# Performance work log

Measured on AMD Instinct MI355X. Metric: run time of the kernel, lower is better.

## Reference

```python
import jax, jax.numpy as jnp
import numpy as np


def setup_inputs() -> dict:
    key = jax.random.key(0)
    k = jax.random.split(key, 6)
    E, F_len, B, r = 64, 128, 1024, 16
    E2 = E * E
    hid = max(1, E2 // r)
    return {
        "mu": jax.random.normal(k[0], (5, B, E, F_len), dtype=jnp.float32),
        "A": jax.random.uniform(k[1], (E, E), dtype=jnp.float32),
        "W1": jax.random.normal(k[2], (hid, E2), dtype=jnp.float32) * 0.02,
        "W2": jax.random.normal(k[3], (E2, hid), dtype=jnp.float32) * 0.02,
        "T1": jax.random.normal(k[4], (5, F_len, F_len), dtype=jnp.float32) * 0.01,
        "T2": jax.random.normal(k[5], (5, F_len, F_len), dtype=jnp.float32) * 0.01,
    }


def reference(mu, A, W1, W2, T1, T2):
    E = A.shape[0]
    # dynamic adjacency: squeeze-excite on flattened A (Linear has no bias)
    h = jax.nn.elu(A.reshape(-1) @ W1.T)          # [E2//r]
    Ad = jax.nn.relu(h @ W2.T).reshape(E, E)       # [E, E]
    # diag(1/rowsum) @ Ad == row-wise normalization (same math, O(E^2))
    D_invA = Ad / jnp.maximum(Ad.sum(axis=1, keepdims=True), 1e-6)
    # per-band chain, vectorized over the 5 bands: elu(D_invA @ elu(m @ T1) @ T2)
    h1 = jax.nn.elu(jnp.einsum('gbef,gfh->gbeh', mu, T1))   # [5,B,E,F]
    h2 = jnp.einsum('xe,gbeh->gbxh', D_invA, h1)            # [5,B,E,F]
    out = jax.nn.elu(jnp.einsum('gbeh,ghf->gbef', h2, T2))  # [5,B,E,F]
    return out
```

## Files before the change

kernel.cpp:

```cpp
#include <hip/hip_runtime.h>
#include <hip/hip_bf16.h>
#include <math.h>

typedef short bf16x8 __attribute__((ext_vector_type(8)));
typedef float f32x4 __attribute__((ext_vector_type(4)));
typedef float float4v __attribute__((ext_vector_type(4)));
typedef unsigned short ushort4v __attribute__((ext_vector_type(4)));

static __device__ __forceinline__ float eluf(float x) {
  float e = __expf(x) - 1.0f;
  return x > 0.f ? x : e;
}
static __device__ __forceinline__ unsigned short f2bf(float f) {
  __hip_bfloat16 h = __float2bfloat16(f);
  return *reinterpret_cast<unsigned short*>(&h);
}
static __device__ __forceinline__ unsigned short f2bf_rne(float f) {
  union { float f; unsigned u; } v; v.f = f;
  unsigned r = v.u + 0x7FFFu + ((v.u >> 16) & 1u);
  return (unsigned short)(r >> 16);
}

__global__ void k_hidden(const float* __restrict__ A, const float* __restrict__ W1,
                         float* __restrict__ hout) {
  int j = blockIdx.x, t = threadIdx.x;
  const float* row = W1 + (size_t)j * 4096;
  float s = 0.f;
  for (int i = t; i < 4096; i += 256) s += A[i] * row[i];
  __shared__ float red[256];
  red[t] = s; __syncthreads();
  for (int off = 128; off > 0; off >>= 1) {
    if (t < off) red[t] += red[t + off];
    __syncthreads();
  }
  if (t == 0) {
    float x = red[0];
    hout[j] = x > 0.f ? x : expm1f(x);
  }
}

__global__ void k_pre2(const float* __restrict__ hbuf, const float* __restrict__ W2,
                       unsigned short* __restrict__ Dout,
                       const float* __restrict__ T1, const float* __restrict__ T2,
                       unsigned short* __restrict__ T1T, unsigned short* __restrict__ T2T) {
  int t = threadIdx.x;
  if (blockIdx.x < 64) {
    int x = blockIdx.x;
    int lane = t & 63, w = t >> 6;
    __shared__ float hs[256];
    __shared__ float ad[64];
    hs[t] = hbuf[t];
    __syncthreads();
    for (int ei = 0; ei < 16; ++ei) {
      int e = w * 16 + ei;
      const float* row = W2 + (size_t)(x * 64 + e) * 256;
      float p = 0.f;
      for (int q = 0; q < 4; ++q) p += row[q * 64 + lane] * hs[q * 64 + lane];
      for (int off = 32; off > 0; off >>= 1) p += __shfl_down(p, off);
      if (lane == 0) ad[e] = fmaxf(p, 0.f);
    }
    __syncthreads();
    if (t < 64) {
      float v = ad[t];
      float rs = v;
      for (int off = 1; off < 64; off <<= 1) rs += __shfl_xor(rs, off);
      Dout[x * 64 + t] = f2bf_rne(v / fmaxf(rs, 1e-6f));
    }
  } else {
    int idx = (blockIdx.x - 64) * 256 + t;
    const float* src = (idx < 81920) ? T1 : T2;
    unsigned short* dst = (idx < 81920) ? T1T : T2T;
    int o = (idx < 81920) ? idx : idx - 81920;
    int g = o >> 14;
    int r = o & 16383;
    int h = r >> 7;
    int f = r & 127;
    dst[o] = f2bf_rne(src[g * 16384 + f * 128 + h]);
  }
}

__launch_bounds__(256, 2)
__global__ void k_main(const float* __restrict__ mu,
                       const unsigned short* __restrict__ Dm,
                       const unsigned short* __restrict__ T1T,
                       const unsigned short* __restrict__ T2T,
                       float* __restrict__ out) {
  __shared__ __align__(16) char smem[49152];
  char* s_h1 = smem + 32768;

  const int g = blockIdx.y, b0 = blockIdx.x * 4;
  const int t = threadIdx.x;
  const int lane = t & 63, w = t >> 6;
  const int l15 = lane & 15, lk = lane >> 4;
  const int nb = w * 32;

  const unsigned short* t1g = T1T + g * 16384;
  const unsigned short* t2g = T2T + g * 16384;
  bf16x8 tb0[4], tb1[4], t2b0[4], t2b1[4];
  #pragma unroll
  for (int kc = 0; kc < 4; ++kc) {
    int k0 = kc * 32 + lk * 8;
    tb0[kc]  = *(const bf16x8*)(const void*)(t1g + (nb + l15) * 128 + k0);
    tb1[kc]  = *(const bf16x8*)(const void*)(t1g + (nb + 16 + l15) * 128 + k0);
    t2b0[kc] = *(const bf16x8*)(const void*)(t2g + (nb + l15) * 128 + k0);
    t2b1[kc] = *(const bf16x8*)(const void*)(t2g + (nb + 16 + l15) * 128 + k0);
  }
  bf16x8 aDf[4][2];
  #pragma unroll
  for (int np = 0; np < 4; ++np)
    #pragma unroll
    for (int kc = 0; kc < 2; ++kc)
      aDf[np][kc] = *(const bf16x8*)(const void*)(Dm + (np * 16 + l15) * 64 + kc * 32 + lk * 8);

  {
    const float4v* src = (const float4v*)(mu + (size_t)(g * 1024 + b0) * 8192);
    #pragma unroll
    for (int k = 0; k < 8; ++k) {
      int q = t + k * 256;
      float4v v = src[q];
      int row = q >> 5, col4 = (q & 31) * 4;
      ushort4v u;
      u[0] = f2bf(v[0]); u[1] = f2bf(v[1]); u[2] = f2bf(v[2]); u[3] = f2bf(v[3]);
      *(ushort4v*)(smem + ((row * 256 + col4 * 2) ^ ((row & 7) << 4))) = u;
    }
  }
  __syncthreads();

  #pragma unroll 1
  for (int it = 0; it < 4; ++it) {
    char* bcur = smem + ((it & 1) << 14);
    char* bnxt = smem + (((it + 1) & 1) << 14);
    const bool pre = (it < 3);

    float4v vn[8];
    if (pre) {
      const float4v* srcn = (const float4v*)(mu + (size_t)(g * 1024 + b0 + it + 1) * 8192);
      #pragma unroll
      for (int k = 0; k < 8; ++k) vn[k] = srcn[t + k * 256];
      __builtin_amdgcn_sched_barrier(0);
    }

    f32x4 acc[4][2];
    #pragma unroll
    for (int m = 0; m < 4; ++m) { acc[m][0] = (f32x4){0,0,0,0}; acc[m][1] = (f32x4){0,0,0,0}; }
    #pragma unroll
    for (int kc = 0; kc < 4; ++kc) {
      int k0 = kc * 32 + lk * 8;
      #pragma unroll
      for (int m = 0; m < 4; ++m) {
        int row = m * 16 + l15;
        bf16x8 a = *(const bf16x8*)(bcur + ((row * 256 + k0 * 2) ^ ((row & 7) << 4)));
        acc[m][0] = __builtin_amdgcn_mfma_f32_16x16x32_bf16(a, tb0[kc], acc[m][0], 0, 0, 0);
        acc[m][1] = __builtin_amdgcn_mfma_f32_16x16x32_bf16(a, tb1[kc], acc[m][1], 0, 0, 0);
      }
    }
    #pragma unroll
    for (int m = 0; m < 4; ++m)
      #pragma unroll
      for (int n = 0; n < 2; ++n) {
        int col = nb + n * 16 + l15;
        int e0 = m * 16 + lk * 4;
        ushort4v u;
        u[0] = f2bf(eluf(acc[m][n][0]));
        u[1] = f2bf(eluf(acc[m][n][1]));
        u[2] = f2bf(eluf(acc[m][n][2]));
        u[3] = f2bf(eluf(acc[m][n][3]));
        *(ushort4v*)(s_h1 + ((col * 128 + e0 * 2) ^ ((col & 7) << 4))) = u;
      }
    __syncthreads();

    f32x4 acc2[2][4];
    #pragma unroll
    for (int mp = 0; mp < 2; ++mp)
      #pragma unroll
      for (int np = 0; np < 4; ++np) acc2[mp][np] = (f32x4){0,0,0,0};
    #pragma unroll
    for (int kc = 0; kc < 2; ++kc) {
      int e0 = kc * 32 + lk * 8;
      int hr0 = w * 32 + l15, hr1 = w * 32 + 16 + l15;
      bf16x8 a0 = *(const bf16x8*)(s_h1 + ((hr0 * 128 + e0 * 2) ^ ((hr0 & 7) << 4)));
      bf16x8 a1 = *(const bf16x8*)(s_h1 + ((hr1 * 128 + e0 * 2) ^ ((hr1 & 7) << 4)));
      #pragma unroll
      for (int np = 0; np < 4; ++np) {
        acc2[0][np] = __builtin_amdgcn_mfma_f32_16x16x32_bf16(a0, aDf[np][kc], acc2[0][np], 0, 0, 0);
        acc2[1][np] = __builtin_amdgcn_mfma_f32_16x16x32_bf16(a1, aDf[np][kc], acc2[1][np], 0, 0, 0);
      }
    }
    #pragma unroll
    for (int mp = 0; mp < 2; ++mp)
      #pragma unroll
      for (int np = 0; np < 4; ++np) {
        int x = np * 16 + l15;
        int h0 = w * 32 + mp * 16 + lk * 4;
        ushort4v u;
        u[0] = f2bf(acc2[mp][np][0]);
        u[1] = f2bf(acc2[mp][np][1]);
        u[2] = f2bf(acc2[mp][np][2]);
        u[3] = f2bf(acc2[mp][np][3]);
        *(ushort4v*)(bcur + ((x * 256 + h0 * 2) ^ ((x & 7) << 4))) = u;
      }
    if (pre) {
      #pragma unroll
      for (int k = 0; k < 8; ++k) {
        int q = t + k * 256;
        int row = q >> 5, col4 = (q & 31) * 4;
        ushort4v u;
        u[0] = f2bf(vn[k][0]); u[1] = f2bf(vn[k][1]);
        u[2] = f2bf(vn[k][2]); u[3] = f2bf(vn[k][3]);
        *(ushort4v*)(bnxt + ((row * 256 + col4 * 2) ^ ((row & 7) << 4))) = u;
      }
    }
    __syncthreads();

    f32x4 acc3[4][2];
    #pragma unroll
    for (int m = 0; m < 4; ++m) { acc3[m][0] = (f32x4){0,0,0,0}; acc3[m][1] = (f32x4){0,0,0,0}; }
    #pragma unroll
    for (int kc = 0; kc < 4; ++kc) {
      int k0 = kc * 32 + lk * 8;
      #pragma unroll
      for (int m = 0; m < 4; ++m) {
        int row = m * 16 + l15;
        bf16x8 a = *(const bf16x8*)(bcur + ((row * 256 + k0 * 2) ^ ((row & 7) << 4)));
        acc3[m][0] = __builtin_amdgcn_mfma_f32_16x16x32_bf16(a, t2b0[kc], acc3[m][0], 0, 0, 0);
        acc3[m][1] = __builtin_amdgcn_mfma_f32_16x16x32_bf16(a, t2b1[kc], acc3[m][1], 0, 0, 0);
      }
    }
    float* ob = out + (size_t)(g * 1024 + b0 + it) * 8192;
    #pragma unroll
    for (int m = 0; m < 4; ++m)
      #pragma unroll
      for (int n = 0; n < 2; ++n) {
        int f = nb + n * 16 + l15;
        #pragma unroll
        for (int r = 0; r < 4; ++r) {
          int e = m * 16 + lk * 4 + r;
          ob[e * 128 + f] = eluf(acc3[m][n][r]);
        }
      }
  }
}

extern "C" void kernel_launch(void* const* d_in, const int* in_sizes, int n_in,
                              void* d_out, int out_size, void* d_ws, size_t ws_size,
                              hipStream_t stream) {
  const float* mu = (const float*)d_in[0];
  const float* A  = (const float*)d_in[1];
  const float* W1 = (const float*)d_in[2];
  const float* W2 = (const float*)d_in[3];
  const float* T1 = (const float*)d_in[4];
  const float* T2 = (const float*)d_in[5];
  float* out = (float*)d_out;

  char* ws = (char*)d_ws;
  float* hbuf          = (float*)ws;
  unsigned short* Dm   = (unsigned short*)(ws + 1024);
  unsigned short* T1T  = (unsigned short*)(ws + 9216);
  unsigned short* T2T  = (unsigned short*)(ws + 173056);

  hipLaunchKernelGGL(k_hidden, dim3(256), dim3(256), 0, stream, A, W1, hbuf);
  hipLaunchKernelGGL(k_pre2,   dim3(704), dim3(256), 0, stream, hbuf, W2, Dm, T1, T2, T1T, T2T);
  hipLaunchKernelGGL(k_main,   dim3(256, 5), dim3(256), 0, stream, mu, Dm, T1T, T2T, out);
}
```

Measured before the change: 101.5 us.

## Keep h1 in registers and feed adjacency MFMA directly, dropping h1 LDS staging

The elu(mu@T1) accumulator fragments are repacked as bf16 B-operands and multiplied by the adjacency with 16x16x16 MFMAs straight from registers. This removes the shared-memory h1 buffer and one barrier. T2 fragments are now loaded per iteration rather than held for the whole kernel, which frees registers and shrinks LDS to 32KB, so launch bounds rise to 3 blocks per CU. The costs are scalar 2-byte LDS stores for the result, repeated T2 global loads, and half-width MFMAs.

```diff
diff --git a/kernel.cpp b/kernel.cpp
--- a/kernel.cpp
+++ b/kernel.cpp
@@ -3,6 +3,7 @@
 #include <math.h>
 
 typedef short bf16x8 __attribute__((ext_vector_type(8)));
+typedef short short4v __attribute__((ext_vector_type(4)));
 typedef float f32x4 __attribute__((ext_vector_type(4)));
 typedef float float4v __attribute__((ext_vector_type(4)));
 typedef unsigned short ushort4v __attribute__((ext_vector_type(4)));
@@ -79,14 +80,13 @@
   }
 }
 
-__launch_bounds__(256, 2)
+__launch_bounds__(256, 3)
 __global__ void k_main(const float* __restrict__ mu,
                        const unsigned short* __restrict__ Dm,
                        const unsigned short* __restrict__ T1T,
                        const unsigned short* __restrict__ T2T,
                        float* __restrict__ out) {
-  __shared__ __align__(16) char smem[49152];
-  char* s_h1 = smem + 32768;
+  __shared__ __align__(16) char smem[32768];
 
   const int g = blockIdx.y, b0 = blockIdx.x * 4;
   const int t = threadIdx.x;
@@ -95,22 +95,19 @@
   const int nb = w * 32;
 
   const unsigned short* t1g = T1T + g * 16384;
-  const unsigned short* t2g = T2T + g * 16384;
-  bf16x8 tb0[4], tb1[4], t2b0[4], t2b1[4];
+  bf16x8 tb0[4], tb1[4];
   #pragma unroll
   for (int kc = 0; kc < 4; ++kc) {
     int k0 = kc * 32 + lk * 8;
-    tb0[kc]  = *(const bf16x8*)(const void*)(t1g + (nb + l15) * 128 + k0);
-    tb1[kc]  = *(const bf16x8*)(const void*)(t1g + (nb + 16 + l15) * 128 + k0);
-    t2b0[kc] = *(const bf16x8*)(const void*)(t2g + (nb + l15) * 128 + k0);
-    t2b1[kc] = *(const bf16x8*)(const void*)(t2g + (nb + 16 + l15) * 128 + k0);
-  }
-  bf16x8 aDf[4][2];
+    tb0[kc] = *(const bf16x8*)(const void*)(t1g + (nb + l15) * 128 + k0);
+    tb1[kc] = *(const bf16x8*)(const void*)(t1g + (nb + 16 + l15) * 128 + k0);
+  }
+  short4v aDf[4][4];
   #pragma unroll
-  for (int np = 0; np < 4; ++np)
-    #pragma unroll
-    for (int kc = 0; kc < 2; ++kc)
-      aDf[np][kc] = *(const bf16x8*)(const void*)(Dm + (np * 16 + l15) * 64 + kc * 32 + lk * 8);
+  for (int mp = 0; mp < 4; ++mp)
+    #pragma unroll
+    for (int kc = 0; kc < 4; ++kc)
+      aDf[mp][kc] = *(const short4v*)(const void*)(Dm + (mp * 16 + l15) * 64 + kc * 16 + lk * 4);
 
   {
     const float4v* src = (const float4v*)(mu + (size_t)(g * 1024 + b0) * 8192);
@@ -154,50 +151,54 @@
         acc[m][1] = __builtin_amdgcn_mfma_f32_16x16x32_bf16(a, tb1[kc], acc[m][1], 0, 0, 0);
       }
     }
+
+    short4v bfr[4][2];
     #pragma unroll
     for (int m = 0; m < 4; ++m)
       #pragma unroll
       for (int n = 0; n < 2; ++n) {
-        int col = nb + n * 16 + l15;
-        int e0 = m * 16 + lk * 4;
-        ushort4v u;
-        u[0] = f2bf(eluf(acc[m][n][0]));
-        u[1] = f2bf(eluf(acc[m][n][1]));
-        u[2] = f2bf(eluf(acc[m][n][2]));
-        u[3] = f2bf(eluf(acc[m][n][3]));
-        *(ushort4v*)(s_h1 + ((col * 128 + e0 * 2) ^ ((col & 7) << 4))) = u;
-      }
-    __syncthreads();
-
-    f32x4 acc2[2][4];
-    #pragma unroll
-    for (int mp = 0; mp < 2; ++mp)
-      #pragma unroll
-      for (int np = 0; np < 4; ++np) acc2[mp][np] = (f32x4){0,0,0,0};
-    #pragma unroll
-    for (int kc = 0; kc < 2; ++kc) {
-      int e0 = kc * 32 + lk * 8;
-      int hr0 = w * 32 + l15, hr1 = w * 32 + 16 + l15;
-      bf16x8 a0 = *(const bf16x8*)(s_h1 + ((hr0 * 128 + e0 * 2) ^ ((hr0 & 7) << 4)));
-      bf16x8 a1 = *(const bf16x8*)(s_h1 + ((hr1 * 128 + e0 * 2) ^ ((hr1 & 7) << 4)));
-      #pragma unroll
-      for (int np = 0; np < 4; ++np) {
-        acc2[0][np] = __builtin_amdgcn_mfma_f32_16x16x32_bf16(a0, aDf[np][kc], acc2[0][np], 0, 0, 0);
-        acc2[1][np] = __builtin_amdgcn_mfma_f32_16x16x32_bf16(a1, aDf[np][kc], acc2[1][np], 0, 0, 0);
-      }
-    }
-    #pragma unroll
-    for (int mp = 0; mp < 2; ++mp)
-      #pragma unroll
-      for (int np = 0; np < 4; ++np) {
-        int x = np * 16 + l15;
-        int h0 = w * 32 + mp * 16 + lk * 4;
-        ushort4v u;
-        u[0] = f2bf(acc2[mp][np][0]);
-        u[1] = f2bf(acc2[mp][np][1]);
-        u[2] = f2bf(acc2[mp][np][2]);
-        u[3] = f2bf(acc2[mp][np][3]);
-        *(ushort4v*)(bcur + ((x * 256 + h0 * 2) ^ ((x & 7) << 4))) = u;
+        short4v s;
+        s[0] = (short)f2bf(eluf(acc[m][n][0]));
+        s[1] = (short)f2bf(eluf(acc[m][n][1]));
+        s[2] = (short)f2bf(eluf(acc[m][n][2]));
+        s[3] = (short)f2bf(eluf(acc[m][n][3]));
+        bfr[m][n] = s;
+      }
+
+    f32x4 acc2[4][2];
+    #pragma unroll
+    for (int mp = 0; mp < 4; ++mp) { acc2[mp][0] = (f32x4){0,0,0,0}; acc2[mp][1] = (f32x4){0,0,0,0}; }
+    #pragma unroll
+    for (int kc = 0; kc < 4; ++kc)
+      #pragma unroll
+      for (int mp = 0; mp < 4; ++mp) {
+        acc2[mp][0] = __builtin_amdgcn_mfma_f32_16x16x16bf16_1k(aDf[mp][kc], bfr[kc][0], acc2[mp][0], 0, 0, 0);
+        acc2[mp][1] = __builtin_amdgcn_mfma_f32_16x16x16bf16_1k(aDf[mp][kc], bfr[kc][1], acc2[mp][1], 0, 0, 0);
+      }
+
+    int t2off = g * 16384;
+    asm volatile("" : "+v"(t2off));
+    const unsigned short* t2g = T2T + t2off;
+    bf16x8 t2b0[4], t2b1[4];
+    #pragma unroll
+    for (int kc = 0; kc < 4; ++kc) {
+      int k0 = kc * 32 + lk * 8;
+      t2b0[kc] = *(const bf16x8*)(const void*)(t2g + (nb + l15) * 128 + k0);
+      t2b1[kc] = *(const bf16x8*)(const void*)(t2g + (nb + 16 + l15) * 128 + k0);
+    }
+
+    __syncthreads();
+
+    #pragma unroll
+    for (int mp = 0; mp < 4; ++mp)
+      #pragma unroll
+      for (int n = 0; n < 2; ++n) {
+        int hc = nb + n * 16 + l15;
+        #pragma unroll
+        for (int r = 0; r < 4; ++r) {
+          int x = mp * 16 + lk * 4 + r;
+          *(unsigned short*)(bcur + ((x * 256 + hc * 2) ^ ((x & 7) << 4))) = f2bf(acc2[mp][n][r]);
+        }
       }
     if (pre) {
       #pragma unroll
```

New measurement: 262.5 us. +158.5%, slower.
